# Kernel tuning notes

Measured on AMD Instinct MI355X. Metric: run time of the kernel, lower is better.

## Reference

```python
import jax, jax.numpy as jnp
import numpy as np

N = 100000        # number of nodes
E = 1600000       # number of edges (avg degree 16)
D_IN = 512
D_OUT = 64


def setup_inputs() -> dict:
    key = jax.random.key(0)
    k1, k2, k3, k4, k5 = jax.random.split(key, 5)
    inputs = jax.random.normal(k1, (N, D_IN), dtype=jnp.float32)
    weight = jax.random.normal(k2, (D_IN, D_OUT), dtype=jnp.float32)
    adj_vals = jax.random.uniform(k3, (E,), dtype=jnp.float32)
    adj_rows = jax.random.randint(k4, (E,), 0, N, dtype=jnp.int32)
    adj_cols = jax.random.randint(k5, (E,), 0, N, dtype=jnp.int32)
    return {
        "inputs": inputs,
        "weight": weight,
        "adj_vals": adj_vals,
        "adj_rows": adj_rows,
        "adj_cols": adj_cols,
    }


def reference(inputs, weight, adj_vals, adj_rows, adj_cols):
    # Dense projection: [N, D_IN] @ [D_IN, D_OUT] -> [N, D_OUT]
    h = inputs @ weight
    # Sparse adjacency spmm (COO): out[r] += vals[e] * h[c] for edge e=(r,c)
    msgs = adj_vals[:, None] * h[adj_cols]            # [E, D_OUT]
    agg = jax.ops.segment_sum(msgs, adj_rows, num_segments=N)  # [N, D_OUT]
    # activation = relu
    return jax.nn.relu(agg)
```

## Files before the change

### kernel.cpp

```cpp
#include <hip/hip_runtime.h>
#include <hip/hip_bf16.h>

#define D_OUT 64
#define K_DIM 512
#define RPB 128
#define RPB_SHIFT 7
#define EPB 8192
#define RCAP 3072

using short8  = __attribute__((ext_vector_type(8))) short;
using floatx4 = __attribute__((ext_vector_type(4))) float;

__device__ inline unsigned short f32_to_bf16(float f) {
    unsigned int u = __float_as_uint(f);
    u += 0x7FFFu + ((u >> 16) & 1u);
    return (unsigned short)(u >> 16);
}

__device__ inline float bf16lo_f32(unsigned int g) {
    return __uint_as_float(g << 16);
}
__device__ inline float bf16hi_f32(unsigned int g) {
    return __uint_as_float(g & 0xFFFF0000u);
}

__global__ void wt_kernel(const float* __restrict__ W, unsigned short* __restrict__ wt) {
    int i = blockIdx.x * blockDim.x + threadIdx.x;
    if (i < D_OUT * K_DIM) {
        int n = i >> 9;
        int k = i & 511;
        wt[i] = f32_to_bf16(W[k * D_OUT + n]);
    }
}

__global__ __launch_bounds__(256) void gemm_kernel(
    const float* __restrict__ A, const unsigned short* __restrict__ wt,
    unsigned short* __restrict__ H, int n) {
    const int tid  = threadIdx.x;
    const int wv   = tid >> 6;
    const int lane = tid & 63;
    const int ln   = lane & 15;
    const int quad = lane >> 4;
    const int row0 = blockIdx.x * 64 + wv * 16;

    int arow = row0 + ln;
    if (arow >= n) arow = n - 1;
    const float* Arow = A + (size_t)arow * K_DIM;
    const unsigned short* wb = wt + (size_t)ln * K_DIM;

    floatx4 acc0 = {0.f, 0.f, 0.f, 0.f};
    floatx4 acc1 = {0.f, 0.f, 0.f, 0.f};
    floatx4 acc2 = {0.f, 0.f, 0.f, 0.f};
    floatx4 acc3 = {0.f, 0.f, 0.f, 0.f};

    for (int h0 = 0; h0 < K_DIM; h0 += 128) {
        float4 t[8];
#pragma unroll
        for (int s = 0; s < 4; s++) {
            t[2 * s]     = *reinterpret_cast<const float4*>(Arow + h0 + s * 32 + quad * 8);
            t[2 * s + 1] = *reinterpret_cast<const float4*>(Arow + h0 + s * 32 + quad * 8 + 4);
        }
        short8 ab[4];
#pragma unroll
        for (int s = 0; s < 4; s++) {
            float4 a0 = t[2 * s], a1 = t[2 * s + 1];
            short8 af;
            af[0] = (short)f32_to_bf16(a0.x);
            af[1] = (short)f32_to_bf16(a0.y);
            af[2] = (short)f32_to_bf16(a0.z);
            af[3] = (short)f32_to_bf16(a0.w);
            af[4] = (short)f32_to_bf16(a1.x);
            af[5] = (short)f32_to_bf16(a1.y);
            af[6] = (short)f32_to_bf16(a1.z);
            af[7] = (short)f32_to_bf16(a1.w);
            ab[s] = af;
        }
#pragma unroll
        for (int s = 0; s < 4; s++) {
            const int ko = h0 + s * 32 + quad * 8;
            short8 b0 = *reinterpret_cast<const short8*>(wb + ko);
            short8 b1 = *reinterpret_cast<const short8*>(wb + 16 * K_DIM + ko);
            short8 b2 = *reinterpret_cast<const short8*>(wb + 32 * K_DIM + ko);
            short8 b3 = *reinterpret_cast<const short8*>(wb + 48 * K_DIM + ko);
            acc0 = __builtin_amdgcn_mfma_f32_16x16x32_bf16(ab[s], b0, acc0, 0, 0, 0);
            acc1 = __builtin_amdgcn_mfma_f32_16x16x32_bf16(ab[s], b1, acc1, 0, 0, 0);
            acc2 = __builtin_amdgcn_mfma_f32_16x16x32_bf16(ab[s], b2, acc2, 0, 0, 0);
            acc3 = __builtin_amdgcn_mfma_f32_16x16x32_bf16(ab[s], b3, acc3, 0, 0, 0);
        }
    }

#pragma unroll
    for (int r = 0; r < 4; r++) {
        int gr = row0 + quad * 4 + r;
        if (gr < n) {
            unsigned short* Hr = H + (size_t)gr * D_OUT;
            Hr[ln]      = f32_to_bf16(acc0[r]);
            Hr[16 + ln] = f32_to_bf16(acc1[r]);
            Hr[32 + ln] = f32_to_bf16(acc2[r]);
            Hr[48 + ln] = f32_to_bf16(acc3[r]);
        }
    }
}

__global__ __launch_bounds__(256) void count_kernel(
    const int* __restrict__ rows, int* __restrict__ counts,
    int E, int nbuck, int nb) {
    extern __shared__ int cnt[];
    const int tid = threadIdx.x, blk = blockIdx.x;
    for (int b = tid; b < nbuck; b += 256) cnt[b] = 0;
    __syncthreads();
    const int base = blk * EPB;
#pragma unroll
    for (int i = 0; i < EPB / 256; i++) {
        int e = base + tid + i * 256;
        if (e < E) atomicAdd(&cnt[rows[e] >> RPB_SHIFT], 1);
    }
    __syncthreads();
    for (int b = tid; b < nbuck; b += 256) counts[b * nb + blk] = cnt[b];
}

__global__ __launch_bounds__(256) void scan1_kernel(
    const int* __restrict__ counts, int* __restrict__ bsum, int n) {
    __shared__ int wsh[4];
    const int tid = threadIdx.x, lane = tid & 63, wid = tid >> 6;
    int i0 = blockIdx.x * 1024 + tid * 4;
    int s = 0;
#pragma unroll
    for (int j = 0; j < 4; j++) {
        int ix = i0 + j;
        s += (ix < n) ? counts[ix] : 0;
    }
#pragma unroll
    for (int d = 32; d; d >>= 1) s += __shfl_xor(s, d, 64);
    if (lane == 0) wsh[wid] = s;
    __syncthreads();
    if (tid == 0) bsum[blockIdx.x] = wsh[0] + wsh[1] + wsh[2] + wsh[3];
}

__global__ __launch_bounds__(1024) void scan2_kernel(
    const int* __restrict__ bsum, int* __restrict__ bbase,
    int* __restrict__ scanned, int nblk, int L, int E) {
    __shared__ int wsum[16];
    const int tid = threadIdx.x, lane = tid & 63, wid = tid >> 6;
    int v = (tid < nblk) ? bsum[tid] : 0;
    int x = v;
#pragma unroll
    for (int d = 1; d < 64; d <<= 1) {
        int y = __shfl_up(x, d, 64);
        if (lane >= d) x += y;
    }
    if (lane == 63) wsum[wid] = x;
    __syncthreads();
    if (tid < 16) {
        int w = wsum[tid];
        int xx = w;
#pragma unroll
        for (int d = 1; d < 16; d <<= 1) {
            int y = __shfl_up(xx, d, 64);
            if (tid >= d) xx += y;
        }
        wsum[tid] = xx - w;
    }
    __syncthreads();
    if (tid < nblk) bbase[tid] = wsum[wid] + (x - v);
    if (tid == 0) scanned[L] = E;
}

__global__ __launch_bounds__(256) void scan3_kernel(
    const int* __restrict__ counts, const int* __restrict__ bbase,
    int* __restrict__ scanned, int n) {
    __shared__ int wsum[4];
    const int tid = threadIdx.x, lane = tid & 63, wid = tid >> 6;
    const int i0 = blockIdx.x * 1024 + tid * 4;
    int v[4];
#pragma unroll
    for (int j = 0; j < 4; j++) {
        int ix = i0 + j;
        v[j] = (ix < n) ? counts[ix] : 0;
    }
#pragma unroll
    for (int j = 1; j < 4; j++) v[j] += v[j - 1];
    int t = v[3];
    int x = t;
#pragma unroll
    for (int d = 1; d < 64; d <<= 1) {
        int y = __shfl_up(x, d, 64);
        if (lane >= d) x += y;
    }
    if (lane == 63) wsum[wid] = x;
    __syncthreads();
    if (tid == 0) {
        int a = 0;
#pragma unroll
        for (int w = 0; w < 4; w++) { int tmp = wsum[w]; wsum[w] = a; a += tmp; }
    }
    __syncthreads();
    int excl = bbase[blockIdx.x] + wsum[wid] + (x - t);
#pragma unroll
    for (int j = 0; j < 4; j++) {
        int ix = i0 + j;
        if (ix < n) scanned[ix] = excl + ((j == 0) ? 0 : v[j - 1]);
    }
}

__global__ __launch_bounds__(256) void partition_kernel(
    const int* __restrict__ rows, const int* __restrict__ cols,
    const float* __restrict__ vals, const int* __restrict__ scanned,
    int2* __restrict__ keys, int E, int nbuck, int nb) {
    extern __shared__ int offs[];
    const int tid = threadIdx.x, blk = blockIdx.x;
    for (int b = tid; b < nbuck; b += 256) offs[b] = scanned[b * nb + blk];
    __syncthreads();
    const int base = blk * EPB;
#pragma unroll
    for (int i = 0; i < EPB / 256; i++) {
        int e = base + tid + i * 256;
        if (e < E) {
            int r = rows[e];
            int c = cols[e];
            float v = vals[e];
            int b = r >> RPB_SHIFT;
            int p = atomicAdd(&offs[b], 1);
            keys[p] = make_int2(c | ((r & (RPB - 1)) << 17), __float_as_int(v));
        }
    }
}

__global__ __launch_bounds__(512) void sort_agg_kernel(
    const unsigned short* __restrict__ h, const int2* __restrict__ keys,
    const int* __restrict__ scanned, float* __restrict__ out,
    int N, int nb) {
    __shared__ int2 rec[RCAP];
    __shared__ int cnt[RPB];
    __shared__ int excl[RPB];
    __shared__ int cur[RPB];
    __shared__ int wtot[2];

    const int tid  = threadIdx.x;
    const int lane = tid & 63;
    const int wv   = tid >> 6;
    const int q    = lane >> 4;
    const int li   = lane & 15;
    const int b    = blockIdx.x;

    const int start = scanned[b * nb];
    const int end   = scanned[(b + 1) * nb];
    const int m     = end - start;

    if (tid < RPB) cnt[tid] = 0;
    __syncthreads();

    for (int i = tid; i < m; i += 512) {
        int rl = keys[start + i].x >> 17;
        atomicAdd(&cnt[rl], 1);
    }
    __syncthreads();

    int v = 0, x = 0;
    if (tid < RPB) {
        v = cnt[tid];
        x = v;
#pragma unroll
        for (int d = 1; d < 64; d <<= 1) {
            int y = __shfl_up(x, d, 64);
            if (lane >= d) x += y;
        }
        if (lane == 63) wtot[tid >> 6] = x;
    }
    __syncthreads();
    if (tid < RPB) {
        int base = (tid >= 64) ? wtot[0] : 0;
        int ex = base + x - v;
        excl[tid] = ex;
        cur[tid]  = ex;
    }
    __syncthreads();

    for (int i = tid; i < m; i += 512) {
        int2 kv = keys[start + i];
        int rl = kv.x >> 17;
        int p = atomicAdd(&cur[rl], 1);
        if (p < RCAP) rec[p] = kv;
    }
    __syncthreads();

    const int row0 = b * RPB;
    for (int rl = wv; rl < RPB; rl += 8) {
        int s = excl[rl];
        int e = cur[rl];
        float4 acc = {0.f, 0.f, 0.f, 0.f};
        int j = s;
        for (; j + 8 <= e; j += 8) {
            int2 kA = rec[j + q];
            int2 kB = rec[j + 4 + q];
            const uint2 gA = *reinterpret_cast<const uint2*>(
                h + (size_t)(kA.x & 0x1FFFF) * D_OUT + li * 4);
            const uint2 gB = *reinterpret_cast<const uint2*>(
                h + (size_t)(kB.x & 0x1FFFF) * D_OUT + li * 4);
            float vA = __int_as_float(kA.y);
            float vB = __int_as_float(kB.y);
            acc.x += vA * bf16lo_f32(gA.x);
            acc.y += vA * bf16hi_f32(gA.x);
            acc.z += vA * bf16lo_f32(gA.y);
            acc.w += vA * bf16hi_f32(gA.y);
            acc.x += vB * bf16lo_f32(gB.x);
            acc.y += vB * bf16hi_f32(gB.x);
            acc.z += vB * bf16lo_f32(gB.y);
            acc.w += vB * bf16hi_f32(gB.y);
        }
        for (; j < e; j += 4) {
            bool on = (j + q) < e;
            int2 kv = rec[on ? j + q : j];
            const uint2 g = *reinterpret_cast<const uint2*>(
                h + (size_t)(kv.x & 0x1FFFF) * D_OUT + li * 4);
            float vv = on ? __int_as_float(kv.y) : 0.f;
            acc.x += vv * bf16lo_f32(g.x);
            acc.y += vv * bf16hi_f32(g.x);
            acc.z += vv * bf16lo_f32(g.y);
            acc.w += vv * bf16hi_f32(g.y);
        }
        acc.x += __shfl_xor(acc.x, 16, 64);
        acc.y += __shfl_xor(acc.y, 16, 64);
        acc.z += __shfl_xor(acc.z, 16, 64);
        acc.w += __shfl_xor(acc.w, 16, 64);
        acc.x += __shfl_xor(acc.x, 32, 64);
        acc.y += __shfl_xor(acc.y, 32, 64);
        acc.z += __shfl_xor(acc.z, 32, 64);
        acc.w += __shfl_xor(acc.w, 32, 64);

        int gr = row0 + rl;
        if (gr < N && q == 0) {
            float4 o;
            o.x = fmaxf(acc.x, 0.f);
            o.y = fmaxf(acc.y, 0.f);
            o.z = fmaxf(acc.z, 0.f);
            o.w = fmaxf(acc.w, 0.f);
            *reinterpret_cast<float4*>(out + (size_t)gr * D_OUT + li * 4) = o;
        }
    }
}

extern "C" void kernel_launch(void* const* d_in, const int* in_sizes, int n_in,
                              void* d_out, int out_size, void* d_ws, size_t ws_size,
                              hipStream_t stream) {
    const float* A    = (const float*)d_in[0];
    const float* W    = (const float*)d_in[1];
    const float* vals = (const float*)d_in[2];
    const int*   rows = (const int*)d_in[3];
    const int*   cols = (const int*)d_in[4];
    float* out = (float*)d_out;

    const int N = out_size / D_OUT;
    const int E = in_sizes[2];
    const int nbuck = (N + RPB - 1) >> RPB_SHIFT;
    const int nb = (E + EPB - 1) / EPB;
    const int L = nbuck * nb;
    const int SB = (L + 1023) / 1024;

    char* ws = (char*)d_ws;
    unsigned short* h       = (unsigned short*)ws;
    int2*           keys    = (int2*)(ws + (size_t)N * D_OUT * 2);
    unsigned short* wt      = (unsigned short*)((char*)keys + (size_t)E * 8);
    int*            counts  = (int*)((char*)wt + (size_t)D_OUT * K_DIM * 2);
    int*            scanned = counts + L;
    int*            bsum    = scanned + L + 1;
    int*            bbase   = bsum + SB;

    const size_t cnt_lds = (size_t)nbuck * 4;

    wt_kernel<<<(D_OUT * K_DIM + 255) / 256, 256, 0, stream>>>(W, wt);
    gemm_kernel<<<(N + 63) / 64, 256, 0, stream>>>(A, wt, h, N);
    count_kernel<<<nb, 256, cnt_lds, stream>>>(rows, counts, E, nbuck, nb);
    scan1_kernel<<<SB, 256, 0, stream>>>(counts, bsum, L);
    scan2_kernel<<<1, 1024, 0, stream>>>(bsum, bbase, scanned, SB, L, E);
    scan3_kernel<<<SB, 256, 0, stream>>>(counts, bbase, scanned, L);
    partition_kernel<<<nb, 256, cnt_lds, stream>>>(rows, cols, vals, scanned, keys, E, nbuck, nb);
    sort_agg_kernel<<<nbuck, 512, 0, stream>>>(h, keys, scanned, out, N, nb);
}
```

Measured before the change: 412.4 us.

## Replace bucketed two-level sort with per-row CSR built by global atomics

Drops the 128-row bucket partition and the in-LDS per-bucket sort. The edge list is now turned into a per-row CSR using global atomic counts, a scan over N rows, and a scatter through global atomic cursors. The aggregation kernel reads each row's edges straight from global memory with a grid-stride over rows. This removes the LDS sort stage and the large counts matrix, but adds heavily contended global atomics and scattered key writes, and the order of edges within a row becomes nondeterministic.

```diff
diff --git a/kernel.cpp b/kernel.cpp
--- a/kernel.cpp
+++ b/kernel.cpp
@@ -3,10 +3,6 @@
 
 #define D_OUT 64
 #define K_DIM 512
-#define RPB 128
-#define RPB_SHIFT 7
-#define EPB 8192
-#define RCAP 3072
 
 using short8  = __attribute__((ext_vector_type(8))) short;
 using floatx4 = __attribute__((ext_vector_type(4))) float;
@@ -102,21 +98,16 @@
     }
 }
 
+__global__ __launch_bounds__(256) void zero_kernel(int* __restrict__ p, int n) {
+    int i = blockIdx.x * 256 + threadIdx.x;
+    if (i < n) p[i] = 0;
+}
+
 __global__ __launch_bounds__(256) void count_kernel(
-    const int* __restrict__ rows, int* __restrict__ counts,
-    int E, int nbuck, int nb) {
-    extern __shared__ int cnt[];
-    const int tid = threadIdx.x, blk = blockIdx.x;
-    for (int b = tid; b < nbuck; b += 256) cnt[b] = 0;
-    __syncthreads();
-    const int base = blk * EPB;
-#pragma unroll
-    for (int i = 0; i < EPB / 256; i++) {
-        int e = base + tid + i * 256;
-        if (e < E) atomicAdd(&cnt[rows[e] >> RPB_SHIFT], 1);
-    }
-    __syncthreads();
-    for (int b = tid; b < nbuck; b += 256) counts[b * nb + blk] = cnt[b];
+    const int* __restrict__ rows, int* __restrict__ counts, int E) {
+    int i = blockIdx.x * 256 + threadIdx.x;
+    const int stride = gridDim.x * 256;
+    for (; i < E; i += stride) atomicAdd(&counts[rows[i]], 1);
 }
 
 __global__ __launch_bounds__(256) void scan1_kernel(
@@ -168,7 +159,7 @@
 
 __global__ __launch_bounds__(256) void scan3_kernel(
     const int* __restrict__ counts, const int* __restrict__ bbase,
-    int* __restrict__ scanned, int n) {
+    int* __restrict__ scanned, int* __restrict__ cursor, int n) {
     __shared__ int wsum[4];
     const int tid = threadIdx.x, lane = tid & 63, wid = tid >> 6;
     const int i0 = blockIdx.x * 1024 + tid * 4;
@@ -199,104 +190,48 @@
 #pragma unroll
     for (int j = 0; j < 4; j++) {
         int ix = i0 + j;
-        if (ix < n) scanned[ix] = excl + ((j == 0) ? 0 : v[j - 1]);
+        if (ix < n) {
+            int e = excl + ((j == 0) ? 0 : v[j - 1]);
+            scanned[ix] = e;
+            cursor[ix]  = e;
+        }
     }
 }
 
 __global__ __launch_bounds__(256) void partition_kernel(
     const int* __restrict__ rows, const int* __restrict__ cols,
-    const float* __restrict__ vals, const int* __restrict__ scanned,
-    int2* __restrict__ keys, int E, int nbuck, int nb) {
-    extern __shared__ int offs[];
-    const int tid = threadIdx.x, blk = blockIdx.x;
-    for (int b = tid; b < nbuck; b += 256) offs[b] = scanned[b * nb + blk];
-    __syncthreads();
-    const int base = blk * EPB;
-#pragma unroll
-    for (int i = 0; i < EPB / 256; i++) {
-        int e = base + tid + i * 256;
-        if (e < E) {
-            int r = rows[e];
-            int c = cols[e];
-            float v = vals[e];
-            int b = r >> RPB_SHIFT;
-            int p = atomicAdd(&offs[b], 1);
-            keys[p] = make_int2(c | ((r & (RPB - 1)) << 17), __float_as_int(v));
-        }
-    }
-}
-
-__global__ __launch_bounds__(512) void sort_agg_kernel(
+    const float* __restrict__ vals, int* __restrict__ cursor,
+    int2* __restrict__ keys, int E) {
+    int i = blockIdx.x * 256 + threadIdx.x;
+    const int stride = gridDim.x * 256;
+    for (; i < E; i += stride) {
+        int r = rows[i];
+        int p = atomicAdd(&cursor[r], 1);
+        keys[p] = make_int2(cols[i], __float_as_int(vals[i]));
+    }
+}
+
+__global__ __launch_bounds__(256) void agg_kernel(
     const unsigned short* __restrict__ h, const int2* __restrict__ keys,
-    const int* __restrict__ scanned, float* __restrict__ out,
-    int N, int nb) {
-    __shared__ int2 rec[RCAP];
-    __shared__ int cnt[RPB];
-    __shared__ int excl[RPB];
-    __shared__ int cur[RPB];
-    __shared__ int wtot[2];
-
-    const int tid  = threadIdx.x;
-    const int lane = tid & 63;
-    const int wv   = tid >> 6;
+    const int* __restrict__ scanned, float* __restrict__ out, int N) {
+    const int lane = threadIdx.x & 63;
     const int q    = lane >> 4;
     const int li   = lane & 15;
-    const int b    = blockIdx.x;
-
-    const int start = scanned[b * nb];
-    const int end   = scanned[(b + 1) * nb];
-    const int m     = end - start;
-
-    if (tid < RPB) cnt[tid] = 0;
-    __syncthreads();
-
-    for (int i = tid; i < m; i += 512) {
-        int rl = keys[start + i].x >> 17;
-        atomicAdd(&cnt[rl], 1);
-    }
-    __syncthreads();
-
-    int v = 0, x = 0;
-    if (tid < RPB) {
-        v = cnt[tid];
-        x = v;
-#pragma unroll
-        for (int d = 1; d < 64; d <<= 1) {
-            int y = __shfl_up(x, d, 64);
-            if (lane >= d) x += y;
-        }
-        if (lane == 63) wtot[tid >> 6] = x;
-    }
-    __syncthreads();
-    if (tid < RPB) {
-        int base = (tid >= 64) ? wtot[0] : 0;
-        int ex = base + x - v;
-        excl[tid] = ex;
-        cur[tid]  = ex;
-    }
-    __syncthreads();
-
-    for (int i = tid; i < m; i += 512) {
-        int2 kv = keys[start + i];
-        int rl = kv.x >> 17;
-        int p = atomicAdd(&cur[rl], 1);
-        if (p < RCAP) rec[p] = kv;
-    }
-    __syncthreads();
-
-    const int row0 = b * RPB;
-    for (int rl = wv; rl < RPB; rl += 8) {
-        int s = excl[rl];
-        int e = cur[rl];
+    int gw = (blockIdx.x * blockDim.x + threadIdx.x) >> 6;
+    const int nw = (gridDim.x * blockDim.x) >> 6;
+
+    for (int r = gw; r < N; r += nw) {
+        const int s = scanned[r];
+        const int e = scanned[r + 1];
         float4 acc = {0.f, 0.f, 0.f, 0.f};
         int j = s;
         for (; j + 8 <= e; j += 8) {
-            int2 kA = rec[j + q];
-            int2 kB = rec[j + 4 + q];
+            int2 kA = keys[j + q];
+            int2 kB = keys[j + 4 + q];
             const uint2 gA = *reinterpret_cast<const uint2*>(
-                h + (size_t)(kA.x & 0x1FFFF) * D_OUT + li * 4);
+                h + (size_t)kA.x * D_OUT + li * 4);
             const uint2 gB = *reinterpret_cast<const uint2*>(
-                h + (size_t)(kB.x & 0x1FFFF) * D_OUT + li * 4);
+                h + (size_t)kB.x * D_OUT + li * 4);
             float vA = __int_as_float(kA.y);
             float vB = __int_as_float(kB.y);
             acc.x += vA * bf16lo_f32(gA.x);
@@ -310,9 +245,9 @@
         }
         for (; j < e; j += 4) {
             bool on = (j + q) < e;
-            int2 kv = rec[on ? j + q : j];
+            int2 kv = keys[on ? j + q : j];
             const uint2 g = *reinterpret_cast<const uint2*>(
-                h + (size_t)(kv.x & 0x1FFFF) * D_OUT + li * 4);
+                h + (size_t)kv.x * D_OUT + li * 4);
             float vv = on ? __int_as_float(kv.y) : 0.f;
             acc.x += vv * bf16lo_f32(g.x);
             acc.y += vv * bf16hi_f32(g.x);
@@ -328,14 +263,13 @@
         acc.z += __shfl_xor(acc.z, 32, 64);
         acc.w += __shfl_xor(acc.w, 32, 64);
 
-        int gr = row0 + rl;
-        if (gr < N && q == 0) {
+        if (q == 0) {
             float4 o;
             o.x = fmaxf(acc.x, 0.f);
             o.y = fmaxf(acc.y, 0.f);
             o.z = fmaxf(acc.z, 0.f);
             o.w = fmaxf(acc.w, 0.f);
-            *reinterpret_cast<float4*>(out + (size_t)gr * D_OUT + li * 4) = o;
+            *reinterpret_cast<float4*>(out + (size_t)r * D_OUT + li * 4) = o;
         }
     }
 }
@@ -352,28 +286,25 @@
 
     const int N = out_size / D_OUT;
     const int E = in_sizes[2];
-    const int nbuck = (N + RPB - 1) >> RPB_SHIFT;
-    const int nb = (E + EPB - 1) / EPB;
-    const int L = nbuck * nb;
-    const int SB = (L + 1023) / 1024;
+    const int SB = (N + 1023) / 1024;
 
     char* ws = (char*)d_ws;
     unsigned short* h       = (unsigned short*)ws;
     int2*           keys    = (int2*)(ws + (size_t)N * D_OUT * 2);
     unsigned short* wt      = (unsigned short*)((char*)keys + (size_t)E * 8);
     int*            counts  = (int*)((char*)wt + (size_t)D_OUT * K_DIM * 2);
-    int*            scanned = counts + L;
-    int*            bsum    = scanned + L + 1;
+    int*            scanned = counts + N;
+    int*            cursor  = scanned + N + 1;
+    int*            bsum    = cursor + N;
     int*            bbase   = bsum + SB;
-
-    const size_t cnt_lds = (size_t)nbuck * 4;
 
     wt_kernel<<<(D_OUT * K_DIM + 255) / 256, 256, 0, stream>>>(W, wt);
     gemm_kernel<<<(N + 63) / 64, 256, 0, stream>>>(A, wt, h, N);
-    count_kernel<<<nb, 256, cnt_lds, stream>>>(rows, counts, E, nbuck, nb);
-    scan1_kernel<<<SB, 256, 0, stream>>>(counts, bsum, L);
-    scan2_kernel<<<1, 1024, 0, stream>>>(bsum, bbase, scanned, SB, L, E);
-    scan3_kernel<<<SB, 256, 0, stream>>>(counts, bbase, scanned, L);
-    partition_kernel<<<nb, 256, cnt_lds, stream>>>(rows, cols, vals, scanned, keys, E, nbuck, nb);
-    sort_agg_kernel<<<nbuck, 512, 0, stream>>>(h, keys, scanned, out, N, nb);
-}
+    zero_kernel<<<(N + 255) / 256, 256, 0, stream>>>(counts, N);
+    count_kernel<<<1024, 256, 0, stream>>>(rows, counts, E);
+    scan1_kernel<<<SB, 256, 0, stream>>>(counts, bsum, N);
+    scan2_kernel<<<1, 1024, 0, stream>>>(bsum, bbase, scanned, SB, N, E);
+    scan3_kernel<<<SB, 256, 0, stream>>>(counts, bbase, scanned, cursor, N);
+    partition_kernel<<<1024, 256, 0, stream>>>(rows, cols, vals, cursor, keys, E);
+    agg_kernel<<<2048, 256, 0, stream>>>(h, keys, scanned, out, N);
+}
```

Result: slower. 548.8 us (+33.1%).

## Replace in-block row sort with LDS float atomic accumulation per bucket

Applied to the files above, without the earlier changes.

The aggregation kernel no longer counts, scans and scatters each bucket's edges into per-row order in LDS. It now streams edges directly and atomically adds scaled gathered features into a 128x64 float accumulator in shared memory, with a lane-dependent rotation of the four components to spread bank conflicts. The relu is applied when the accumulator is written out. This removes two passes over the keys and several barriers, but relies on LDS float atomics, whose contention and throughput may cost more than the register accumulation they replace. Summation order also becomes nondeterministic.

```diff
diff --git a/kernel.cpp b/kernel.cpp
--- a/kernel.cpp
+++ b/kernel.cpp
@@ -6,7 +6,6 @@
 #define RPB 128
 #define RPB_SHIFT 7
 #define EPB 8192
-#define RCAP 3072
 
 using short8  = __attribute__((ext_vector_type(8))) short;
 using floatx4 = __attribute__((ext_vector_type(4))) float;
@@ -226,117 +225,77 @@
     }
 }
 
-__global__ __launch_bounds__(512) void sort_agg_kernel(
+__global__ __launch_bounds__(512) void agg_kernel(
     const unsigned short* __restrict__ h, const int2* __restrict__ keys,
     const int* __restrict__ scanned, float* __restrict__ out,
     int N, int nb) {
-    __shared__ int2 rec[RCAP];
-    __shared__ int cnt[RPB];
-    __shared__ int excl[RPB];
-    __shared__ int cur[RPB];
-    __shared__ int wtot[2];
-
-    const int tid  = threadIdx.x;
-    const int lane = tid & 63;
-    const int wv   = tid >> 6;
-    const int q    = lane >> 4;
-    const int li   = lane & 15;
-    const int b    = blockIdx.x;
+    __shared__ float acc[RPB * D_OUT];
+
+    const int tid = threadIdx.x;
+    const int g   = tid >> 4;
+    const int li  = tid & 15;
+    const int b   = blockIdx.x;
 
     const int start = scanned[b * nb];
     const int end   = scanned[(b + 1) * nb];
     const int m     = end - start;
 
-    if (tid < RPB) cnt[tid] = 0;
-    __syncthreads();
-
-    for (int i = tid; i < m; i += 512) {
-        int rl = keys[start + i].x >> 17;
-        atomicAdd(&cnt[rl], 1);
-    }
-    __syncthreads();
-
-    int v = 0, x = 0;
-    if (tid < RPB) {
-        v = cnt[tid];
-        x = v;
-#pragma unroll
-        for (int d = 1; d < 64; d <<= 1) {
-            int y = __shfl_up(x, d, 64);
-            if (lane >= d) x += y;
-        }
-        if (lane == 63) wtot[tid >> 6] = x;
-    }
-    __syncthreads();
-    if (tid < RPB) {
-        int base = (tid >= 64) ? wtot[0] : 0;
-        int ex = base + x - v;
-        excl[tid] = ex;
-        cur[tid]  = ex;
-    }
-    __syncthreads();
-
-    for (int i = tid; i < m; i += 512) {
+    for (int i = tid; i < RPB * D_OUT; i += 512) acc[i] = 0.f;
+    __syncthreads();
+
+    const bool r2 = (g & 2) != 0;
+    const bool r1 = (g & 1) != 0;
+
+    int i = g;
+    for (; i + 32 < m; i += 64) {
+        int2 kA = keys[start + i];
+        int2 kB = keys[start + i + 32];
+        const uint2 gA = *reinterpret_cast<const uint2*>(
+            h + (size_t)(kA.x & 0x1FFFF) * D_OUT + li * 4);
+        const uint2 gB = *reinterpret_cast<const uint2*>(
+            h + (size_t)(kB.x & 0x1FFFF) * D_OUT + li * 4);
+        float vA = __int_as_float(kA.y);
+        float vB = __int_as_float(kB.y);
+        float a0 = vA * bf16lo_f32(gA.x), a1 = vA * bf16hi_f32(gA.x);
+        float a2 = vA * bf16lo_f32(gA.y), a3 = vA * bf16hi_f32(gA.y);
+        float b0 = vB * bf16lo_f32(gB.x), b1 = vB * bf16hi_f32(gB.x);
+        float b2 = vB * bf16lo_f32(gB.y), b3 = vB * bf16hi_f32(gB.y);
+        float tA0 = r2 ? a2 : a0, tA1 = r2 ? a3 : a1, tA2 = r2 ? a0 : a2, tA3 = r2 ? a1 : a3;
+        float wA0 = r1 ? tA1 : tA0, wA1 = r1 ? tA2 : tA1, wA2 = r1 ? tA3 : tA2, wA3 = r1 ? tA0 : tA3;
+        float tB0 = r2 ? b2 : b0, tB1 = r2 ? b3 : b1, tB2 = r2 ? b0 : b2, tB3 = r2 ? b1 : b3;
+        float wB0 = r1 ? tB1 : tB0, wB1 = r1 ? tB2 : tB1, wB2 = r1 ? tB3 : tB2, wB3 = r1 ? tB0 : tB3;
+        const int baseA = (kA.x >> 17) * D_OUT + li * 4;
+        const int baseB = (kB.x >> 17) * D_OUT + li * 4;
+        atomicAdd(&acc[baseA + ((0 + g) & 3)], wA0);
+        atomicAdd(&acc[baseB + ((0 + g) & 3)], wB0);
+        atomicAdd(&acc[baseA + ((1 + g) & 3)], wA1);
+        atomicAdd(&acc[baseB + ((1 + g) & 3)], wB1);
+        atomicAdd(&acc[baseA + ((2 + g) & 3)], wA2);
+        atomicAdd(&acc[baseB + ((2 + g) & 3)], wB2);
+        atomicAdd(&acc[baseA + ((3 + g) & 3)], wA3);
+        atomicAdd(&acc[baseB + ((3 + g) & 3)], wB3);
+    }
+    for (; i < m; i += 32) {
         int2 kv = keys[start + i];
-        int rl = kv.x >> 17;
-        int p = atomicAdd(&cur[rl], 1);
-        if (p < RCAP) rec[p] = kv;
+        const uint2 gv = *reinterpret_cast<const uint2*>(
+            h + (size_t)(kv.x & 0x1FFFF) * D_OUT + li * 4);
+        float v = __int_as_float(kv.y);
+        float a0 = v * bf16lo_f32(gv.x), a1 = v * bf16hi_f32(gv.x);
+        float a2 = v * bf16lo_f32(gv.y), a3 = v * bf16hi_f32(gv.y);
+        float t0 = r2 ? a2 : a0, t1 = r2 ? a3 : a1, t2 = r2 ? a0 : a2, t3 = r2 ? a1 : a3;
+        float w0 = r1 ? t1 : t0, w1 = r1 ? t2 : t1, w2 = r1 ? t3 : t2, w3 = r1 ? t0 : t3;
+        const int ba = (kv.x >> 17) * D_OUT + li * 4;
+        atomicAdd(&acc[ba + ((0 + g) & 3)], w0);
+        atomicAdd(&acc[ba + ((1 + g) & 3)], w1);
+        atomicAdd(&acc[ba + ((2 + g) & 3)], w2);
+        atomicAdd(&acc[ba + ((3 + g) & 3)], w3);
     }
     __syncthreads();
 
     const int row0 = b * RPB;
-    for (int rl = wv; rl < RPB; rl += 8) {
-        int s = excl[rl];
-        int e = cur[rl];
-        float4 acc = {0.f, 0.f, 0.f, 0.f};
-        int j = s;
-        for (; j + 8 <= e; j += 8) {
-            int2 kA = rec[j + q];
-            int2 kB = rec[j + 4 + q];
-            const uint2 gA = *reinterpret_cast<const uint2*>(
-                h + (size_t)(kA.x & 0x1FFFF) * D_OUT + li * 4);
-            const uint2 gB = *reinterpret_cast<const uint2*>(
-                h + (size_t)(kB.x & 0x1FFFF) * D_OUT + li * 4);
-            float vA = __int_as_float(kA.y);
-            float vB = __int_as_float(kB.y);
-            acc.x += vA * bf16lo_f32(gA.x);
-            acc.y += vA * bf16hi_f32(gA.x);
-            acc.z += vA * bf16lo_f32(gA.y);
-            acc.w += vA * bf16hi_f32(gA.y);
-            acc.x += vB * bf16lo_f32(gB.x);
-            acc.y += vB * bf16hi_f32(gB.x);
-            acc.z += vB * bf16lo_f32(gB.y);
-            acc.w += vB * bf16hi_f32(gB.y);
-        }
-        for (; j < e; j += 4) {
-            bool on = (j + q) < e;
-            int2 kv = rec[on ? j + q : j];
-            const uint2 g = *reinterpret_cast<const uint2*>(
-                h + (size_t)(kv.x & 0x1FFFF) * D_OUT + li * 4);
-            float vv = on ? __int_as_float(kv.y) : 0.f;
-            acc.x += vv * bf16lo_f32(g.x);
-            acc.y += vv * bf16hi_f32(g.x);
-            acc.z += vv * bf16lo_f32(g.y);
-            acc.w += vv * bf16hi_f32(g.y);
-        }
-        acc.x += __shfl_xor(acc.x, 16, 64);
-        acc.y += __shfl_xor(acc.y, 16, 64);
-        acc.z += __shfl_xor(acc.z, 16, 64);
-        acc.w += __shfl_xor(acc.w, 16, 64);
-        acc.x += __shfl_xor(acc.x, 32, 64);
-        acc.y += __shfl_xor(acc.y, 32, 64);
-        acc.z += __shfl_xor(acc.z, 32, 64);
-        acc.w += __shfl_xor(acc.w, 32, 64);
-
-        int gr = row0 + rl;
-        if (gr < N && q == 0) {
-            float4 o;
-            o.x = fmaxf(acc.x, 0.f);
-            o.y = fmaxf(acc.y, 0.f);
-            o.z = fmaxf(acc.z, 0.f);
-            o.w = fmaxf(acc.w, 0.f);
-            *reinterpret_cast<float4*>(out + (size_t)gr * D_OUT + li * 4) = o;
-        }
+    for (int idx = tid; idx < RPB * D_OUT; idx += 512) {
+        int r = row0 + (idx >> 6);
+        if (r < N) out[(size_t)r * D_OUT + (idx & 63)] = fmaxf(acc[idx], 0.f);
     }
 }
 
@@ -375,5 +334,5 @@
     scan2_kernel<<<1, 1024, 0, stream>>>(bsum, bbase, scanned, SB, L, E);
     scan3_kernel<<<SB, 256, 0, stream>>>(counts, bbase, scanned, L);
     partition_kernel<<<nb, 256, cnt_lds, stream>>>(rows, cols, vals, scanned, keys, E, nbuck, nb);
-    sort_agg_kernel<<<nbuck, 512, 0, stream>>>(h, keys, scanned, out, N, nb);
-}
+    agg_kernel<<<nbuck, 512, 0, stream>>>(h, keys, scanned, out, N, nb);
+}
```

New measurement: 1.054 ms. 156% more time.
